# Performance work log

Measured on AMD Instinct MI355X. Metric: run time of the kernel, lower is better.

The kernel has to match this reference:

```python
import jax, jax.numpy as jnp
from jax import lax
import numpy as np

B, C, L = 64, 32, 1549
HID = 256          # LSTM hidden per direction
NH, DK = 8, 64     # n_heads, d_k ; NH*DK = 2*HID = 512
D2 = 2 * HID


def setup_inputs() -> dict:
    key = jax.random.key(0)
    ks = jax.random.split(key, 32)
    r = lambda i, shape: jax.random.normal(ks[i], shape, jnp.float32) * 0.05
    inp = {"x": jax.random.normal(ks[0], (B, C, L), jnp.float32)}
    inp["conv_w"] = r(1, (C, C, 16))
    inp["conv_b"] = r(2, (C,))
    inp["bn_gamma"] = 1.0 + r(3, (C,))
    inp["bn_beta"] = r(4, (C,))
    inp["bn_mean"] = r(5, (C,))
    inp["bn_var"] = jax.random.uniform(ks[6], (C,), jnp.float32, 0.5, 1.5)
    names = [("W_ih0f", (4*HID, C)), ("W_hh0f", (4*HID, HID)), ("b0f", (4*HID,)),
             ("W_ih0b", (4*HID, C)), ("W_hh0b", (4*HID, HID)), ("b0b", (4*HID,)),
             ("W_ih1f", (4*HID, D2)), ("W_hh1f", (4*HID, HID)), ("b1f", (4*HID,)),
             ("W_ih1b", (4*HID, D2)), ("W_hh1b", (4*HID, HID)), ("b1b", (4*HID,)),
             ("Wq", (D2, D2)), ("bq", (D2,)), ("Wk", (D2, D2)), ("bk", (D2,)),
             ("Wv", (D2, D2)), ("bv", (D2,)), ("ln_g", (D2,)), ("ln_b", (D2,)),
             ("fc_w", (1, D2)), ("fc_b", (1,))]
    for j, (n, s) in enumerate(names):
        inp[n] = r(7 + j, s)
    inp["ln_g"] = 1.0 + inp["ln_g"]
    return inp


def _lstm_dir(xg, W_hh, reverse):
    # xg: [B,S,4H] precomputed input-to-gate projections (+biases); PyTorch gate order i,f,g,o
    if reverse:
        xg = xg[:, ::-1]
    Bq = xg.shape[0]
    H = W_hh.shape[1]
    def step(carry, g_t):
        h, c = carry
        g = g_t + h @ W_hh.T
        i, f, gg, o = jnp.split(g, 4, axis=-1)
        c = jax.nn.sigmoid(f) * c + jax.nn.sigmoid(i) * jnp.tanh(gg)
        h = jax.nn.sigmoid(o) * jnp.tanh(c)
        return (h, c), h
    init = (jnp.zeros((Bq, H), xg.dtype), jnp.zeros((Bq, H), xg.dtype))
    _, hs = lax.scan(step, init, jnp.swapaxes(xg, 0, 1))
    hs = jnp.swapaxes(hs, 0, 1)
    return hs[:, ::-1] if reverse else hs


def _bilstm(x, Wif, Whf, bf, Wib, Whb, bb):
    hf = _lstm_dir(jnp.einsum('bsd,gd->bsg', x, Wif) + bf, Whf, False)
    hb = _lstm_dir(jnp.einsum('bsd,gd->bsg', x, Wib) + bb, Whb, True)
    return jnp.concatenate([hf, hb], axis=-1)


def _forward(x, conv_w, conv_b, bn_gamma, bn_beta, bn_mean, bn_var,
             W_ih0f, W_hh0f, b0f, W_ih0b, W_hh0b, b0b,
             W_ih1f, W_hh1f, b1f, W_ih1b, W_hh1b, b1b,
             Wq, bq, Wk, bk, Wv, bv, ln_g, ln_b, fc_w, fc_b):
    # conv1d (k=16, pad=1) + BatchNorm (eval) + relu + maxpool(k=3, stride=3)
    h = lax.conv_general_dilated(x, conv_w, (1,), [(1, 1)],
                                 dimension_numbers=('NCH', 'OIH', 'NCH')) + conv_b[None, :, None]
    h = (h - bn_mean[None, :, None]) * jax.lax.rsqrt(bn_var[None, :, None] + 1e-5) \
        * bn_gamma[None, :, None] + bn_beta[None, :, None]
    h = jax.nn.relu(h)
    h = lax.reduce_window(h, -jnp.inf, lax.max, (1, 1, 3), (1, 1, 3), 'VALID')
    h = jnp.transpose(h, (0, 2, 1))            # [B, S, C]
    # 2-layer bidirectional LSTM (eval: inter-layer dropout inactive)
    out = _bilstm(h, W_ih0f, W_hh0f, b0f, W_ih0b, W_hh0b, b0b)
    out = _bilstm(out, W_ih1f, W_hh1f, b1f, W_ih1b, W_hh1b, b1b)   # [B, S, 512]
    Bq, S, _ = out.shape
    q = (out @ Wq.T + bq).reshape(Bq, S, NH, DK).transpose(0, 2, 1, 3)
    k = (out @ Wk.T + bk).reshape(Bq, S, NH, DK).transpose(0, 2, 1, 3)
    v = (out @ Wv.T + bv).reshape(Bq, S, NH, DK).transpose(0, 2, 1, 3)
    attn = jnp.einsum('bhsd,bhtd->bhst', q, k) / np.sqrt(DK)
    # NOTE: original uses nn.LogSoftmax(dim=1) -> log-softmax over the HEAD axis
    la = jax.nn.log_softmax(attn, axis=1)
    ctx = jnp.einsum('bhst,bhtd->bhsd', la, v)
    ctx = jnp.transpose(ctx, (0, 2, 1, 3)).reshape(Bq, S, D2)
    r = out + ctx
    mu = jnp.mean(r, axis=-1, keepdims=True)
    var = jnp.mean((r - mu) ** 2, axis=-1, keepdims=True)
    r = (r - mu) * jax.lax.rsqrt(var + 1e-5) * ln_g + ln_b
    pooled = jnp.mean(r, axis=1)               # len_reduction='mean'
    return pooled @ fc_w.T + fc_b              # [B, 1]


def reference(x, conv_w, conv_b, bn_gamma, bn_beta, bn_mean, bn_var,
              W_ih0f, W_hh0f, b0f, W_ih0b, W_hh0b, b0b,
              W_ih1f, W_hh1f, b1f, W_ih1b, W_hh1b, b1b,
              Wq, bq, Wk, bk, Wv, bv, ln_g, ln_b, fc_w, fc_b):
    return _forward(x, conv_w, conv_b, bn_gamma, bn_beta, bn_mean, bn_var,
                    W_ih0f, W_hh0f, b0f, W_ih0b, W_hh0b, b0b,
                    W_ih1f, W_hh1f, b1f, W_ih1b, W_hh1b, b1b,
                    Wq, bq, Wk, bk, Wv, bv, ln_g, ln_b, fc_w, fc_b)
```

## Files before the change

### kernel.cpp

```cpp
#include <hip/hip_runtime.h>
#include <hip/hip_bf16.h>
#include <math.h>

#define L_IN 1549
#define S_OUT 512

typedef __hip_bfloat16 bf16;
typedef __attribute__((ext_vector_type(8))) short bfrag;
typedef __attribute__((ext_vector_type(4))) float f32x4;

__device__ __forceinline__ float bfbits2f(unsigned short u) {
    union { unsigned int i; float f; } x;
    x.i = ((unsigned int)u) << 16;
    return x.f;
}
__device__ __forceinline__ unsigned short f2bfbits(float f) {
    union { float f; unsigned int i; } x; x.f = f;
    unsigned int lsb = (x.i >> 16) & 1;
    return (unsigned short)((x.i + 0x7fff + lsb) >> 16);
}

__device__ __forceinline__ float fast_sig(float x) {
    float e = __builtin_amdgcn_exp2f(-1.442695041f * x);
    return __builtin_amdgcn_rcpf(1.f + e);
}
__device__ __forceinline__ float fast_tanh(float x) {
    float e = __builtin_amdgcn_exp2f(2.885390082f * x);
    return 1.f - 2.f * __builtin_amdgcn_rcpf(1.f + e);
}

#if __has_builtin(__builtin_amdgcn_fdot2_f32_bf16)
typedef __attribute__((ext_vector_type(2))) __bf16 v2bf;
__device__ __forceinline__ float dot2bf(unsigned int w, unsigned int h, float c) {
    union { unsigned int u; v2bf v; } a, b;
    a.u = w; b.u = h;
    return __builtin_amdgcn_fdot2_f32_bf16(a.v, b.v, c, false);
}
#else
__device__ __forceinline__ float dot2bf(unsigned int w, unsigned int h, float c) {
    union { unsigned int i; float f; } w0, w1, h0, h1;
    w0.i = w << 16; w1.i = w & 0xffff0000u;
    h0.i = h << 16; h1.i = h & 0xffff0000u;
    return c + w0.f * h0.f + w1.f * h1.f;
}
#endif

__global__ __launch_bounds__(256) void conv_bn_pool(
    const float* __restrict__ x, const float* __restrict__ w,
    const float* __restrict__ cb, const float* __restrict__ gamma,
    const float* __restrict__ beta, const float* __restrict__ mean,
    const float* __restrict__ var, bf16* __restrict__ h0)
{
    int b  = blockIdx.y;
    int sg = blockIdx.x;
    __shared__ float xs[32][40];
    int tid = threadIdx.x;
    int base = sg * 24;
    for (int i = tid; i < 32 * 40; i += 256) {
        int ci = i / 40, dl = i % 40;
        int l = base - 1 + dl;
        xs[ci][dl] = (l >= 0 && l < L_IN) ? x[(size_t)(b * 32 + ci) * L_IN + l] : 0.f;
    }
    __syncthreads();
    int c = tid & 31, sl = tid >> 5;
    float scale = gamma[c] * rsqrtf(var[c] + 1e-5f);
    float shift = beta[c] - mean[c] * scale;
    float bias = cb[c];
    float acc0 = bias, acc1 = bias, acc2 = bias;
    int off0 = 3 * sl;
    for (int ci = 0; ci < 32; ++ci) {
        const float* wrp = w + (size_t)(c * 32 + ci) * 16;
        float4 w0 = *(const float4*)(wrp);
        float4 w1 = *(const float4*)(wrp + 4);
        float4 w2 = *(const float4*)(wrp + 8);
        float4 w3 = *(const float4*)(wrp + 12);
        float wk[16] = {w0.x, w0.y, w0.z, w0.w, w1.x, w1.y, w1.z, w1.w,
                        w2.x, w2.y, w2.z, w2.w, w3.x, w3.y, w3.z, w3.w};
        const float* xr = &xs[ci][off0];
        #pragma unroll
        for (int kk = 0; kk < 16; ++kk) {
            float xv0 = xr[kk];
            float xv1 = xr[kk + 1];
            float xv2 = xr[kk + 2];
            acc0 += xv0 * wk[kk];
            acc1 += xv1 * wk[kk];
            acc2 += xv2 * wk[kk];
        }
    }
    float y0 = fmaxf(acc0 * scale + shift, 0.f);
    float y1 = fmaxf(acc1 * scale + shift, 0.f);
    float y2 = fmaxf(acc2 * scale + shift, 0.f);
    float best = fmaxf(fmaxf(y0, y1), y2);
    int s = sg * 8 + sl;
    h0[((size_t)b * S_OUT + s) * 32 + c] = __float2bfloat16(best);
}

__global__ __launch_bounds__(256) void pack_all(
    const float* __restrict__ Wh0, const float* __restrict__ Wh1,
    const float* __restrict__ Wh2, const float* __restrict__ Wh3,
    const float* __restrict__ A0, const float* __restrict__ A1,
    const float* __restrict__ A2, const float* __restrict__ A3,
    const float* __restrict__ A4, const float* __restrict__ A5,
    const float* __restrict__ A6,
    unsigned int* __restrict__ wl, unsigned short* __restrict__ wpk)
{
    int idx = blockIdx.x * 256 + threadIdx.x;
    if (idx < 524288) {
        int set = idx >> 17;
        int i = idx & 131071;
        const float* W = (set == 0) ? Wh0 : (set == 1) ? Wh1 : (set == 2) ? Wh2 : Wh3;
        int kpl, j;
        if (i < 102400) {
            kpl = i >> 11; j = i & 2047;
        } else if (i < 116736) {
            int m = i - 102400;
            kpl = 50 + (m >> 11); j = m & 2047;
        } else {
            int m = i - 116736;
            kpl = 57 + (m >> 11); j = m & 2047;
        }
        int t = j >> 2, gi = j & 3;
        int g = 4 * (t & 255) + gi;
        int kp = (t >> 8) * 64 + kpl;
        unsigned int lo = f2bfbits(W[(size_t)g * 256 + 2 * kp]);
        unsigned int hi = f2bfbits(W[(size_t)g * 256 + 2 * kp + 1]);
        wl[(size_t)set * 131072 + i] = lo | (hi << 16);
    } else {
        int i = idx - 524288;
        const float* src; int j;
        if      (i <   32768) { src = A0; j = i; }
        else if (i <   65536) { src = A1; j = i - 32768; }
        else if (i <  589824) { src = A2; j = i - 65536; }
        else if (i < 1114112) { src = A3; j = i - 589824; }
        else if (i < 1376256) { src = A4; j = i - 1114112; }
        else if (i < 1638400) { src = A5; j = i - 1376256; }
        else if (i < 1900544) { src = A6; j = i - 1638400; }
        else return;
        wpk[i] = f2bfbits(src[j]);
    }
}

#define LDA 40
__global__ __launch_bounds__(256) void gemm_mfma(
    const bf16* __restrict__ A,
    const bf16* __restrict__ Bm0, const bf16* __restrict__ Bm1, const bf16* __restrict__ Bm2,
    const float* __restrict__ bs0, const float* __restrict__ bs1, const float* __restrict__ bs2,
    bf16* __restrict__ Cm0, bf16* __restrict__ Cm1, bf16* __restrict__ Cm2,
    int M, int N, int K)
{
    int nbn = N >> 7;
    int nbm = M >> 7;
    int lid = blockIdx.x;
    int xcd = lid & 7;
    int slot = lid >> 3;
    int bn = slot % nbn;
    int pair = xcd + 8 * (slot / nbn);
    int bm = pair % nbm;
    int z  = pair / nbm;

    const bf16* B = (z == 0) ? Bm0 : ((z == 1) ? Bm1 : Bm2);
    const float* bias = (z == 0) ? bs0 : ((z == 1) ? bs1 : bs2);
    bf16* C = (z == 0) ? Cm0 : ((z == 1) ? Cm1 : Cm2);

    __shared__ bf16 As[128 * LDA];
    __shared__ bf16 Bs[128 * LDA];

    int tid = threadIdx.x;
    int lane = tid & 63;
    int wave = tid >> 6;
    int wm = (wave >> 1) * 64;
    int wn = (wave & 1) * 64;

    int sr = tid >> 2;
    int sc = (tid & 3) * 8;
    const bf16* Ag = A + (size_t)(bm * 128 + sr) * K + sc;
    const bf16* Bg = B + (size_t)(bn * 128 + sr) * K + sc;

    int fm = lane & 15;
    int fk = (lane >> 4) * 8;

    f32x4 acc[4][4];
    #pragma unroll
    for (int i = 0; i < 4; ++i)
        #pragma unroll
        for (int j = 0; j < 4; ++j) acc[i][j] = (f32x4)(0.f);

    for (int k0 = 0; k0 < K; k0 += 32) {
        float4 a0 = *(const float4*)(Ag + k0);
        float4 a1 = *(const float4*)(Ag + (size_t)64 * K + k0);
        float4 b0 = *(const float4*)(Bg + k0);
        float4 b1 = *(const float4*)(Bg + (size_t)64 * K + k0);
        __syncthreads();
        *(float4*)(As + sr * LDA + sc)        = a0;
        *(float4*)(As + (sr + 64) * LDA + sc) = a1;
        *(float4*)(Bs + sr * LDA + sc)        = b0;
        *(float4*)(Bs + (sr + 64) * LDA + sc) = b1;
        __syncthreads();

        bfrag af[4], bfr[4];
        #pragma unroll
        for (int i = 0; i < 4; ++i)
            af[i] = *(const bfrag*)(As + (wm + i * 16 + fm) * LDA + fk);
        #pragma unroll
        for (int j = 0; j < 4; ++j)
            bfr[j] = *(const bfrag*)(Bs + (wn + j * 16 + fm) * LDA + fk);
        #pragma unroll
        for (int i = 0; i < 4; ++i)
            #pragma unroll
            for (int j = 0; j < 4; ++j)
                acc[i][j] = __builtin_amdgcn_mfma_f32_16x16x32_bf16(
                    af[i], bfr[j], acc[i][j], 0, 0, 0);
    }

    int rbase = (lane >> 4) * 4;
    #pragma unroll
    for (int j = 0; j < 4; ++j) {
        int n = bn * 128 + wn + j * 16 + (lane & 15);
        float bv = bias[n];
        #pragma unroll
        for (int i = 0; i < 4; ++i) {
            #pragma unroll
            for (int r = 0; r < 4; ++r) {
                int m = bm * 128 + wm + i * 16 + rbase + r;
                C[(size_t)m * N + n] = __float2bfloat16(acc[i][j][r] + bv);
            }
        }
    }
}

__global__ __launch_bounds__(512, 2) void lstm_reg(
    const bf16* __restrict__ xg_f, const bf16* __restrict__ xg_b,
    const unsigned int* __restrict__ Wl, bf16* __restrict__ out)
{
    int u = blockIdx.x;
    int b = u & 63, dir = u >> 6;
    const unsigned int* W = Wl + (size_t)dir * 131072;
    const bf16* xg = dir ? xg_b : xg_f;
    int t = threadIdx.x;

    __shared__ unsigned int lw[14336];
    __shared__ __align__(16) unsigned int hsb[2][128];
    __shared__ __align__(16) float gsh[2][1024];

    unsigned int wr[200];
    #pragma unroll
    for (int j = 0; j < 50; ++j)
        *(uint4*)&wr[j * 4] = *(const uint4*)&W[j * 2048 + 4 * t];
    for (int i = t; i < 14336; i += 512) lw[i] = W[102400 + i];
    if (t < 128) { hsb[0][t] = 0u; }
    float cst = 0.f;
    __syncthreads();

    const unsigned int* Wst = W + 116736;
    int par = 0;
    int khalf = t >> 8;
    int gq = t & 255;
    const unsigned int* lwp = lw + 4 * t;
    unsigned short hb = 0;
    size_t oaddr = 0;

    for (int step = 0; step < 512; ++step) {
        int ts = dir ? (511 - step) : step;

        uint4 sv[7];
        #pragma unroll
        for (int s = 0; s < 7; ++s)
            sv[s] = *(const uint4*)&Wst[s * 2048 + 4 * t];
        uint2 xv = make_uint2(0u, 0u);
        if (khalf == 0)
            xv = *(const uint2*)(xg + ((size_t)b * 512 + ts) * 1024 + 4 * t);

        const unsigned int* hs = hsb[par] + khalf * 64;
        float a0 = 0.f, a1 = 0.f, a2 = 0.f, a3 = 0.f;
        #pragma unroll
        for (int q = 0; q < 16; ++q) {
            uint4 hv = *(const uint4*)&hs[q * 4];
            #pragma unroll
            for (int r = 0; r < 4; ++r) {
                int kpl = q * 4 + r;
                unsigned int h2 = (&hv.x)[r];
                if (kpl < 50) {
                    const unsigned int* w4 = &wr[kpl * 4];
                    a0 = dot2bf(w4[0], h2, a0);
                    a1 = dot2bf(w4[1], h2, a1);
                    a2 = dot2bf(w4[2], h2, a2);
                    a3 = dot2bf(w4[3], h2, a3);
                } else if (kpl < 57) {
                    uint4 wv = *(const uint4*)&lwp[(kpl - 50) * 2048];
                    a0 = dot2bf(wv.x, h2, a0);
                    a1 = dot2bf(wv.y, h2, a1);
                    a2 = dot2bf(wv.z, h2, a2);
                    a3 = dot2bf(wv.w, h2, a3);
                } else {
                    uint4 wv = sv[kpl - 57];
                    a0 = dot2bf(wv.x, h2, a0);
                    a1 = dot2bf(wv.y, h2, a1);
                    a2 = dot2bf(wv.z, h2, a2);
                    a3 = dot2bf(wv.w, h2, a3);
                }
            }
        }
        if (khalf == 0) {
            a0 += bfbits2f((unsigned short)(xv.x & 0xffff));
            a1 += bfbits2f((unsigned short)(xv.x >> 16));
            a2 += bfbits2f((unsigned short)(xv.y & 0xffff));
            a3 += bfbits2f((unsigned short)(xv.y >> 16));
        }

        *(float4*)&gsh[khalf][4 * gq] = make_float4(a0, a1, a2, a3);
        __syncthreads();

        bool act = (t < 256);
        if (act) {
            float gi = gsh[0][t]       + gsh[1][t];
            float gf = gsh[0][256 + t] + gsh[1][256 + t];
            float gg = gsh[0][512 + t] + gsh[1][512 + t];
            float go = gsh[0][768 + t] + gsh[1][768 + t];
            float si = fast_sig(gi);
            float sf = fast_sig(gf);
            float so = fast_sig(go);
            cst = sf * cst + si * fast_tanh(gg);
            float h = so * fast_tanh(cst);
            hb = f2bfbits(h);
            ((unsigned short*)hsb[par ^ 1])[t] = hb;
            oaddr = ((size_t)b * 512 + ts) * 512 + dir * 256 + t;
        }
        __syncthreads();
        if (act) *(unsigned short*)(out + oaddr) = hb;
        par ^= 1;
    }
}

__global__ __launch_bounds__(256) void vt_transpose(
    const bf16* __restrict__ v, bf16* __restrict__ vt)
{
    __shared__ unsigned short tile[64 * 73];
    int b = blockIdx.z;
    int s0 = blockIdx.x * 64, n0 = blockIdx.y * 64;
    int tid = threadIdx.x;
    #pragma unroll
    for (int u = 0; u < 2; ++u) {
        int idx = tid + u * 256;
        int si = idx >> 3, nj = (idx & 7) << 3;
        bfrag val = *(const bfrag*)(v + ((size_t)(b * 512 + s0 + si)) * 512 + n0 + nj);
        #pragma unroll
        for (int jj = 0; jj < 8; ++jj)
            tile[(nj + jj) * 73 + si] = ((unsigned short*)&val)[jj];
    }
    __syncthreads();
    #pragma unroll
    for (int u = 0; u < 2; ++u) {
        int idx = tid + u * 256;
        int ni = idx >> 3, sj = (idx & 7) << 3;
        unsigned short outv[8];
        #pragma unroll
        for (int jj = 0; jj < 8; ++jj)
            outv[jj] = tile[ni * 73 + sj + jj];
        *(float4*)(vt + (size_t)b * 262144 + (size_t)(n0 + ni) * 512 + s0 + sj) =
            *(float4*)outv;
    }
}

__global__ __launch_bounds__(256, 2) void attention_mfma(
    const bf16* __restrict__ q, const bf16* __restrict__ k,
    const bf16* __restrict__ vt, bf16* r)
{
    int n_ = blockIdx.x;
    int xcd = n_ & 7;
    int slot = n_ >> 3;
    int b = xcd + ((slot >> 4) << 3);
    int s0 = (slot & 15) * 32;
    int tid = threadIdx.x;
    int wave = tid >> 6;
    int sw = wave & 1, dh = wave >> 1;
    int lane = tid & 63;
    int L15 = lane & 15, quad = lane >> 4;

    const bf16* qrow = q + ((size_t)(b * 512 + s0 + sw * 16 + L15)) * 512;
    bfrag qf[8][2];
    #pragma unroll
    for (int h = 0; h < 8; ++h) {
        qf[h][0] = *(const bfrag*)(qrow + h * 64 + quad * 8);
        qf[h][1] = *(const bfrag*)(qrow + h * 64 + 32 + quad * 8);
    }

    f32x4 ctxa[8][2];
    #pragma unroll
    for (int h = 0; h < 8; ++h) {
        ctxa[h][0] = (f32x4)(0.f);
        ctxa[h][1] = (f32x4)(0.f);
    }

    int tperm = ((L15 >> 2) << 3) + (L15 & 3);
    const bf16* kbase = k + (size_t)(b * 512) * 512;
    const bf16* vbase = vt + (size_t)b * 262144;

    for (int tc = 0; tc < 512; tc += 32) {
        f32x4 sa[8][2];
        #pragma unroll
        for (int h = 0; h < 8; ++h) {
            #pragma unroll
            for (int tile = 0; tile < 2; ++tile) {
                const bf16* krow = kbase
                    + (size_t)(tc + tile * 4 + tperm) * 512 + h * 64 + quad * 8;
                bfrag a0 = *(const bfrag*)(krow);
                bfrag a1 = *(const bfrag*)(krow + 32);
                f32x4 acc = __builtin_amdgcn_mfma_f32_16x16x32_bf16(
                    a0, qf[h][0], (f32x4)(0.f), 0, 0, 0);
                acc = __builtin_amdgcn_mfma_f32_16x16x32_bf16(
                    a1, qf[h][1], acc, 0, 0, 0);
                sa[h][tile] = acc;
            }
        }
        bfrag pf[8];
        #pragma unroll
        for (int tile = 0; tile < 2; ++tile) {
            #pragma unroll
            for (int rr = 0; rr < 4; ++rr) {
                float sc[8];
                float m = -1e30f;
                #pragma unroll
                for (int h = 0; h < 8; ++h) {
                    sc[h] = sa[h][tile][rr] * 0.125f;
                    m = fmaxf(m, sc[h]);
                }
                float sum = 0.f;
                #pragma unroll
                for (int h = 0; h < 8; ++h)
                    sum += __builtin_amdgcn_exp2f((sc[h] - m) * 1.442695041f);
                float lse = m + 0.6931471806f * __builtin_amdgcn_logf(sum);
                #pragma unroll
                for (int h = 0; h < 8; ++h)
                    ((unsigned short*)&pf[h])[tile * 4 + rr] = f2bfbits(sc[h] - lse);
            }
        }
        #pragma unroll
        for (int h = 0; h < 8; ++h) {
            #pragma unroll
            for (int dt = 0; dt < 2; ++dt) {
                int n = h * 64 + dh * 32 + dt * 16 + L15;
                bfrag vf = *(const bfrag*)(vbase + (size_t)n * 512 + tc + quad * 8);
                ctxa[h][dt] = __builtin_amdgcn_mfma_f32_16x16x32_bf16(
                    pf[h], vf, ctxa[h][dt], 0, 0, 0);
            }
        }
    }
    #pragma unroll
    for (int h = 0; h < 8; ++h) {
        #pragma unroll
        for (int dt = 0; dt < 2; ++dt) {
            int n = h * 64 + dh * 32 + dt * 16 + L15;
            #pragma unroll
            for (int rr = 0; rr < 4; ++rr) {
                size_t addr =
                    ((size_t)(b * 512 + s0 + sw * 16 + quad * 4 + rr)) * 512 + n;
                float o = __bfloat162float(r[addr]);
                r[addr] = __float2bfloat16(o + ctxa[h][dt][rr]);
            }
        }
    }
}

__global__ __launch_bounds__(512) void ln_pool_fc(
    const bf16* __restrict__ r, const float* __restrict__ g, const float* __restrict__ bt,
    const float* __restrict__ fcw, const float* __restrict__ fcb, float* __restrict__ out)
{
    int b = blockIdx.y;
    int s = blockIdx.x * 8 + (threadIdx.x >> 6);
    int lane = threadIdx.x & 63;
    int n0 = lane * 8;

    float gf[8];
    float btf = 0.f;
    #pragma unroll
    for (int j = 0; j < 8; ++j) {
        float fw = fcw[n0 + j];
        gf[j] = g[n0 + j] * fw;
        btf += bt[n0 + j] * fw;
    }

    bfrag rv = *(const bfrag*)(r + ((size_t)(b * 512 + s)) * 512 + n0);
    float v[8];
    float s1 = 0.f, s2 = 0.f;
    #pragma unroll
    for (int j = 0; j < 8; ++j) {
        v[j] = bfbits2f(((const unsigned short*)&rv)[j]);
        s1 += v[j];
        s2 += v[j] * v[j];
    }
    #pragma unroll
    for (int off = 32; off > 0; off >>= 1) {
        s1 += __shfl_xor(s1, off);
        s2 += __shfl_xor(s2, off);
    }
    float mu = s1 * (1.f / 512.f);
    float var = s2 * (1.f / 512.f) - mu * mu;
    float rs = rsqrtf(var + 1e-5f);

    float d = 0.f;
    #pragma unroll
    for (int j = 0; j < 8; ++j) d += (v[j] - mu) * gf[j];
    #pragma unroll
    for (int off = 32; off > 0; off >>= 1) {
        d += __shfl_down(d, off);
        btf += __shfl_down(btf, off);
    }
    if (lane == 0) {
        float val = d * rs * (1.f / 512.f);
        if (s == 0) val += btf + fcb[0];
        atomicAdd(out + b, val);
    }
}

extern "C" void kernel_launch(void* const* d_in, const int* in_sizes, int n_in,
                              void* d_out, int out_size, void* d_ws, size_t ws_size,
                              hipStream_t stream)
{
    (void)in_sizes; (void)n_in; (void)ws_size;
    const float* x      = (const float*)d_in[0];
    const float* conv_w = (const float*)d_in[1];
    const float* conv_b = (const float*)d_in[2];
    const float* bn_g   = (const float*)d_in[3];
    const float* bn_b   = (const float*)d_in[4];
    const float* bn_m   = (const float*)d_in[5];
    const float* bn_v   = (const float*)d_in[6];
    const float* W_ih0f = (const float*)d_in[7];
    const float* W_hh0f = (const float*)d_in[8];
    const float* b0f    = (const float*)d_in[9];
    const float* W_ih0b = (const float*)d_in[10];
    const float* W_hh0b = (const float*)d_in[11];
    const float* b0b    = (const float*)d_in[12];
    const float* W_ih1f = (const float*)d_in[13];
    const float* W_hh1f = (const float*)d_in[14];
    const float* b1f    = (const float*)d_in[15];
    const float* W_ih1b = (const float*)d_in[16];
    const float* W_hh1b = (const float*)d_in[17];
    const float* b1b    = (const float*)d_in[18];
    const float* Wq = (const float*)d_in[19];
    const float* bq = (const float*)d_in[20];
    const float* Wk = (const float*)d_in[21];
    const float* bk = (const float*)d_in[22];
    const float* Wv = (const float*)d_in[23];
    const float* bv = (const float*)d_in[24];
    const float* ln_g = (const float*)d_in[25];
    const float* ln_b = (const float*)d_in[26];
    const float* fc_w = (const float*)d_in[27];
    const float* fc_b = (const float*)d_in[28];
    float* out = (float*)d_out;

    char* ws = (char*)d_ws;
    bf16* xgf  = (bf16*)ws;
    bf16* xgb  = xgf + 33554432;
    bf16* out0 = (bf16*)(ws + 134217728);
    bf16* out1 = (bf16*)(ws + 167772160);
    bf16* h0   = (bf16*)(ws + 201326592);
    unsigned int* wl0 = (unsigned int*)(ws + 203423744);
    unsigned int* wl1 = wl0 + 262144;
    bf16* wpk  = (bf16*)(ws + 205520896);
    bf16* qb = xgf;
    bf16* kb = xgf + 16777216;
    bf16* vb = xgb;
    bf16* vtb = out0;

    hipMemsetAsync(d_out, 0, (size_t)out_size * sizeof(float), stream);

    pack_all<<<9472, 256, 0, stream>>>(
        W_hh0f, W_hh0b, W_hh1f, W_hh1b,
        W_ih0f, W_ih0b, W_ih1f, W_ih1b, Wq, Wk, Wv,
        wl0, (unsigned short*)wpk);

    conv_bn_pool<<<dim3(64, 64), 256, 0, stream>>>(
        x, conv_w, conv_b, bn_g, bn_b, bn_m, bn_v, h0);

    gemm_mfma<<<4096, 256, 0, stream>>>(
        h0, wpk, wpk + 32768, nullptr, b0f, b0b, nullptr, xgf, xgb, nullptr,
        32768, 1024, 32);

    lstm_reg<<<128, 512, 0, stream>>>(xgf, xgb, wl0, out0);

    gemm_mfma<<<4096, 256, 0, stream>>>(
        out0, wpk + 65536, wpk + 589824, nullptr, b1f, b1b, nullptr,
        xgf, xgb, nullptr, 32768, 1024, 512);

    lstm_reg<<<128, 512, 0, stream>>>(xgf, xgb, wl1, out1);

    gemm_mfma<<<3072, 256, 0, stream>>>(
        out1, wpk + 1114112, wpk + 1376256, wpk + 1638400, bq, bk, bv,
        qb, kb, vb, 32768, 512, 512);

    vt_transpose<<<dim3(8, 8, 64), 256, 0, stream>>>(vb, vtb);

    attention_mfma<<<1024, 256, 0, stream>>>(qb, kb, vtb, out1);

    ln_pool_fc<<<dim3(64, 64), 512, 0, stream>>>(out1, ln_g, ln_b, fc_w, fc_b, out);
}
```

Before: 2.730 ms.

## Split LSTM recurrence across 1024 threads with two gate columns each

New measurement: 3.899 ms. +42.8%, slower.

```diff
diff --git a/kernel.cpp b/kernel.cpp
--- a/kernel.cpp
+++ b/kernel.cpp
@@ -119,9 +119,9 @@
             int m = i - 116736;
             kpl = 57 + (m >> 11); j = m & 2047;
         }
-        int t = j >> 2, gi = j & 3;
-        int g = 4 * (t & 255) + gi;
-        int kp = (t >> 8) * 64 + kpl;
+        int t = j >> 1, col = j & 1;
+        int g = 2 * (t & 511) + col;
+        int kp = (t >> 9) * 64 + kpl;
         unsigned int lo = f2bfbits(W[(size_t)g * 256 + 2 * kp]);
         unsigned int hi = f2bfbits(W[(size_t)g * 256 + 2 * kp + 1]);
         wl[(size_t)set * 131072 + i] = lo | (hi << 16);
@@ -228,7 +228,7 @@
     }
 }
 
-__global__ __launch_bounds__(512, 2) void lstm_reg(
+__global__ __launch_bounds__(1024, 1) void lstm_reg(
     const bf16* __restrict__ xg_f, const bf16* __restrict__ xg_b,
     const unsigned int* __restrict__ Wl, bf16* __restrict__ out)
 {
@@ -242,36 +242,36 @@
     __shared__ __align__(16) unsigned int hsb[2][128];
     __shared__ __align__(16) float gsh[2][1024];
 
-    unsigned int wr[200];
+    unsigned int wr[100];
     #pragma unroll
     for (int j = 0; j < 50; ++j)
-        *(uint4*)&wr[j * 4] = *(const uint4*)&W[j * 2048 + 4 * t];
-    for (int i = t; i < 14336; i += 512) lw[i] = W[102400 + i];
+        *(uint2*)&wr[j * 2] = *(const uint2*)&W[j * 2048 + 2 * t];
+    for (int i = t; i < 14336; i += 1024) lw[i] = W[102400 + i];
     if (t < 128) { hsb[0][t] = 0u; }
     float cst = 0.f;
     __syncthreads();
 
     const unsigned int* Wst = W + 116736;
     int par = 0;
-    int khalf = t >> 8;
-    int gq = t & 255;
-    const unsigned int* lwp = lw + 4 * t;
+    int khalf = t >> 9;
+    int gp = t & 511;
+    const unsigned int* lwp = lw + 2 * t;
     unsigned short hb = 0;
     size_t oaddr = 0;
 
     for (int step = 0; step < 512; ++step) {
         int ts = dir ? (511 - step) : step;
 
-        uint4 sv[7];
+        uint2 sv[7];
         #pragma unroll
         for (int s = 0; s < 7; ++s)
-            sv[s] = *(const uint4*)&Wst[s * 2048 + 4 * t];
-        uint2 xv = make_uint2(0u, 0u);
+            sv[s] = *(const uint2*)&Wst[s * 2048 + 2 * t];
+        unsigned int xv = 0u;
         if (khalf == 0)
-            xv = *(const uint2*)(xg + ((size_t)b * 512 + ts) * 1024 + 4 * t);
+            xv = *(const unsigned int*)(xg + ((size_t)b * 512 + ts) * 1024 + 2 * gp);
 
         const unsigned int* hs = hsb[par] + khalf * 64;
-        float a0 = 0.f, a1 = 0.f, a2 = 0.f, a3 = 0.f;
+        float a0 = 0.f, a1 = 0.f, e0 = 0.f, e1 = 0.f;
         #pragma unroll
         for (int q = 0; q < 16; ++q) {
             uint4 hv = *(const uint4*)&hs[q * 4];
@@ -279,35 +279,29 @@
             for (int r = 0; r < 4; ++r) {
                 int kpl = q * 4 + r;
                 unsigned int h2 = (&hv.x)[r];
+                float& d0 = (r & 1) ? e0 : a0;
+                float& d1 = (r & 1) ? e1 : a1;
                 if (kpl < 50) {
-                    const unsigned int* w4 = &wr[kpl * 4];
-                    a0 = dot2bf(w4[0], h2, a0);
-                    a1 = dot2bf(w4[1], h2, a1);
-                    a2 = dot2bf(w4[2], h2, a2);
-                    a3 = dot2bf(w4[3], h2, a3);
+                    d0 = dot2bf(wr[kpl * 2], h2, d0);
+                    d1 = dot2bf(wr[kpl * 2 + 1], h2, d1);
                 } else if (kpl < 57) {
-                    uint4 wv = *(const uint4*)&lwp[(kpl - 50) * 2048];
-                    a0 = dot2bf(wv.x, h2, a0);
-                    a1 = dot2bf(wv.y, h2, a1);
-                    a2 = dot2bf(wv.z, h2, a2);
-                    a3 = dot2bf(wv.w, h2, a3);
+                    uint2 wv = *(const uint2*)&lwp[(kpl - 50) * 2048];
+                    d0 = dot2bf(wv.x, h2, d0);
+                    d1 = dot2bf(wv.y, h2, d1);
                 } else {
-                    uint4 wv = sv[kpl - 57];
-                    a0 = dot2bf(wv.x, h2, a0);
-                    a1 = dot2bf(wv.y, h2, a1);
-                    a2 = dot2bf(wv.z, h2, a2);
-                    a3 = dot2bf(wv.w, h2, a3);
+                    uint2 wv = sv[kpl - 57];
+                    d0 = dot2bf(wv.x, h2, d0);
+                    d1 = dot2bf(wv.y, h2, d1);
                 }
             }
         }
+        a0 += e0; a1 += e1;
         if (khalf == 0) {
-            a0 += bfbits2f((unsigned short)(xv.x & 0xffff));
-            a1 += bfbits2f((unsigned short)(xv.x >> 16));
-            a2 += bfbits2f((unsigned short)(xv.y & 0xffff));
-            a3 += bfbits2f((unsigned short)(xv.y >> 16));
-        }
-
-        *(float4*)&gsh[khalf][4 * gq] = make_float4(a0, a1, a2, a3);
+            a0 += bfbits2f((unsigned short)(xv & 0xffff));
+            a1 += bfbits2f((unsigned short)(xv >> 16));
+        }
+
+        *(float2*)&gsh[khalf][2 * gp] = make_float2(a0, a1);
         __syncthreads();
 
         bool act = (t < 256);
@@ -576,13 +570,13 @@
         h0, wpk, wpk + 32768, nullptr, b0f, b0b, nullptr, xgf, xgb, nullptr,
         32768, 1024, 32);
 
-    lstm_reg<<<128, 512, 0, stream>>>(xgf, xgb, wl0, out0);
+    lstm_reg<<<128, 1024, 0, stream>>>(xgf, xgb, wl0, out0);
 
     gemm_mfma<<<4096, 256, 0, stream>>>(
         out0, wpk + 65536, wpk + 589824, nullptr, b1f, b1b, nullptr,
         xgf, xgb, nullptr, 32768, 1024, 512);
 
-    lstm_reg<<<128, 512, 0, stream>>>(xgf, xgb, wl1, out1);
+    lstm_reg<<<128, 1024, 0, stream>>>(xgf, xgb, wl1, out1);
 
     gemm_mfma<<<3072, 256, 0, stream>>>(
         out1, wpk + 1114112, wpk + 1376256, wpk + 1638400, bq, bk, bv,
```
